# Kernel optimization log

Measured on AMD Instinct MI355X. Metric: run time of the kernel, lower is better.

Reference implementation:

```python
import jax, jax.numpy as jnp
import numpy as np

B, T, C = 8, 1024, 2048  # batch, seq_len (<= T_MAX=1024), n_embd == dim_att


def setup_inputs() -> dict:
    key = jax.random.key(0)
    ks = jax.random.split(key, 10)
    inp = {
        "x": jax.random.normal(ks[0], (B, T, C), dtype=jnp.float32),
        "time_decay": jax.random.normal(ks[1], (C,), dtype=jnp.float32),
        "time_first": jax.random.normal(ks[2], (C,), dtype=jnp.float32),
        "time_mix_k": jax.random.uniform(ks[3], (C,), dtype=jnp.float32),
        "time_mix_v": jax.random.uniform(ks[4], (C,), dtype=jnp.float32),
        "time_mix_r": jax.random.uniform(ks[5], (C,), dtype=jnp.float32),
        "Wk": jax.random.normal(ks[6], (C, C), dtype=jnp.float32) / np.sqrt(C),
        "Wv": jax.random.normal(ks[7], (C, C), dtype=jnp.float32) / np.sqrt(C),
        "Wr": jax.random.normal(ks[8], (C, C), dtype=jnp.float32) / np.sqrt(C),
        "Wo": jax.random.normal(ks[9], (C, C), dtype=jnp.float32) / np.sqrt(C),
    }
    return inp


def _wkv(time_decay, time_first, k, v):
    # Numerically-stabilized RWKV linear-attention recurrence (rwkv_linear_attention_cpu).
    # k, v: [B, T, C]; state tracked in float32.
    w = -jnp.exp(time_decay.astype(jnp.float32))  # [C]
    u = time_first.astype(jnp.float32)            # [C]
    kf = k.astype(jnp.float32)
    vf = v.astype(jnp.float32)

    def step(carry, kv):
        num, den, mx = carry           # each [B, C]
        kt, vt = kv                    # each [B, C]
        max_out = jnp.maximum(mx, kt + u)
        e1 = jnp.exp(mx - max_out)
        e2 = jnp.exp(kt + u - max_out)
        out = (e1 * num + e2 * vt) / (e1 * den + e2)
        max_st = jnp.maximum(mx + w, kt)
        e1s = jnp.exp(mx + w - max_st)
        e2s = jnp.exp(kt - max_st)
        return (e1s * num + e2s * vt, e1s * den + e2s, max_st), out

    Bn, Tn, Cn = k.shape
    init = (jnp.zeros((Bn, Cn), jnp.float32),
            jnp.zeros((Bn, Cn), jnp.float32),
            jnp.full((Bn, Cn), -1e38, jnp.float32))
    kT = jnp.swapaxes(kf, 0, 1)  # [T, B, C]
    vT = jnp.swapaxes(vf, 0, 1)
    _, outs = jax.lax.scan(step, init, (kT, vT))
    return jnp.swapaxes(outs, 0, 1).astype(k.dtype)  # [B, T, C]


def reference(x, time_decay, time_first, time_mix_k, time_mix_v, time_mix_r, Wk, Wv, Wr, Wo):
    # time_shift: shift sequence right by one, zero at t=0
    shifted = jnp.pad(x, ((0, 0), (1, 0), (0, 0)))[:, :-1]
    xk = x * time_mix_k + shifted * (1.0 - time_mix_k)
    xv = x * time_mix_v + shifted * (1.0 - time_mix_v)
    xr = x * time_mix_r + shifted * (1.0 - time_mix_r)
    k = jnp.einsum('btc,dc->btd', xk, Wk)
    v = jnp.einsum('btc,dc->btd', xv, Wv)
    r = jnp.einsum('btc,dc->btd', xr, Wr)
    sr = jax.nn.sigmoid(r)
    rwkv = _wkv(time_decay, time_first, k, v)
    return jnp.einsum('btd,cd->btc', sr * rwkv, Wo)
```

## Files before the change

kernel.cpp:

```cpp
#include <hip/hip_runtime.h>
#include <stdint.h>

#define B_DIM 8
#define T_DIM 1024
#define C_DIM 2048
#define M_DIM (B_DIM * T_DIM)
#define SEG   32
#define SEGL  (T_DIM / SEG)

typedef __bf16 bf16x8 __attribute__((ext_vector_type(8)));
typedef __bf16 bf16x4 __attribute__((ext_vector_type(4)));
typedef float  f32x4  __attribute__((ext_vector_type(4)));

__device__ __forceinline__ void gld_lds16(const void* g, void* l) {
    __builtin_amdgcn_global_load_lds((__attribute__((address_space(1))) void*)g,
                                     (__attribute__((address_space(3))) void*)l,
                                     16, 0, 0);
}

__global__ __launch_bounds__(256) void cast_w_kernel(
    const float* __restrict__ w0, const float* __restrict__ w1,
    const float* __restrict__ w2, const float* __restrict__ w3,
    __bf16* __restrict__ dst) {
    const float* srcs[4] = {w0, w1, w2, w3};
    const float* s = srcs[blockIdx.y];
    __bf16* d = dst + (size_t)blockIdx.y * (size_t)C_DIM * C_DIM;
    const size_t i = ((size_t)blockIdx.x * 256 + threadIdx.x) * 4;
    f32x4 v = *(const f32x4*)(s + i);
    bf16x4 o;
#pragma unroll
    for (int j = 0; j < 4; ++j) o[j] = (__bf16)v[j];
    *(bf16x4*)(d + i) = o;
}

__global__ __launch_bounds__(256) void mix4_kernel(
    const float* __restrict__ x,
    const float* __restrict__ mk, const float* __restrict__ mv,
    const float* __restrict__ mr,
    __bf16* __restrict__ xk, __bf16* __restrict__ xv, __bf16* __restrict__ xr) {
    const size_t idx = ((size_t)blockIdx.x * 256 + threadIdx.x) * 4;
    const int c = (int)(idx & (C_DIM - 1));
    const int t = (int)((idx >> 11) & (T_DIM - 1));

    f32x4 xc = *(const f32x4*)(x + idx);
    f32x4 sh = {0.f, 0.f, 0.f, 0.f};
    if (t != 0) sh = *(const f32x4*)(x + idx - C_DIM);
    f32x4 k4 = *(const f32x4*)(mk + c);
    f32x4 v4 = *(const f32x4*)(mv + c);
    f32x4 r4 = *(const f32x4*)(mr + c);

    bf16x4 ok, ov, orr;
#pragma unroll
    for (int j = 0; j < 4; ++j) {
        float xx = xc[j], ss = sh[j];
        ok[j]  = (__bf16)(xx * k4[j] + ss * (1.f - k4[j]));
        ov[j]  = (__bf16)(xx * v4[j] + ss * (1.f - v4[j]));
        orr[j] = (__bf16)(xx * r4[j] + ss * (1.f - r4[j]));
    }
    *(bf16x4*)(xk + idx) = ok;
    *(bf16x4*)(xv + idx) = ov;
    *(bf16x4*)(xr + idx) = orr;
}

#define VMCNT(N) asm volatile("s_waitcnt vmcnt(" #N ")" ::: "memory")
#define LGKM0()  do { asm volatile("s_waitcnt lgkmcnt(0)" ::: "memory"); \
                      __builtin_amdgcn_sched_barrier(0); } while (0)

#define MFMA4(mi, a)                                                              \
    acc[mi][0] = __builtin_amdgcn_mfma_f32_16x16x32_bf16(a, b0, acc[mi][0], 0, 0, 0); \
    acc[mi][1] = __builtin_amdgcn_mfma_f32_16x16x32_bf16(a, b1, acc[mi][1], 0, 0, 0); \
    acc[mi][2] = __builtin_amdgcn_mfma_f32_16x16x32_bf16(a, b2, acc[mi][2], 0, 0, 0); \
    acc[mi][3] = __builtin_amdgcn_mfma_f32_16x16x32_bf16(a, b3, acc[mi][3], 0, 0, 0)

#define STAGE_A(TT, NB)                                                           \
    do { const __bf16* g_ = Ag + (TT) * 32;                                       \
         __bf16* l_ = lA + (NB) * 8192;                                           \
         gld_lds16(g_, l_);                                                       \
         gld_lds16(g_ + (size_t)128 * C_DIM, l_ + 4096); } while (0)

#define STAGE_B(TT, NB)                                                           \
    do { const __bf16* g_ = Bg + (TT) * 32;                                       \
         __bf16* l_ = lB + (NB) * 8192;                                           \
         gld_lds16(g_, l_);                                                       \
         gld_lds16(g_ + (size_t)128 * C_DIM, l_ + 4096); } while (0)

#define GBLOCK(BUF, DO_STAGE, TT, DO_VM, VM)                                      \
  { const char* pa = fA + (BUF) * 16384;                                          \
    const char* pb = fB + (BUF) * 16384;                                          \
    bf16x8 af0 = *(const bf16x8*)(pa);                                            \
    bf16x8 af1 = *(const bf16x8*)(pa + 1024);                                     \
    bf16x8 af2 = *(const bf16x8*)(pa + 2048);                                     \
    bf16x8 af3 = *(const bf16x8*)(pa + 3072);                                     \
    bf16x8 b0  = *(const bf16x8*)(pb);                                            \
    bf16x8 b1  = *(const bf16x8*)(pb + 1024);                                     \
    bf16x8 b2  = *(const bf16x8*)(pb + 2048);                                     \
    bf16x8 b3  = *(const bf16x8*)(pb + 3072);                                     \
    if (DO_STAGE) { STAGE_A(TT, ((BUF) + 3) & 3); }                               \
    __builtin_amdgcn_s_barrier();                                                 \
    LGKM0();                                                                      \
    __builtin_amdgcn_s_setprio(1);                                                \
    MFMA4(0, af0); MFMA4(1, af1); MFMA4(2, af2); MFMA4(3, af3);                   \
    __builtin_amdgcn_s_setprio(0);                                                \
    __builtin_amdgcn_s_barrier();                                                 \
    af0 = *(const bf16x8*)(pa + 4096);                                            \
    af1 = *(const bf16x8*)(pa + 5120);                                            \
    af2 = *(const bf16x8*)(pa + 6144);                                            \
    af3 = *(const bf16x8*)(pa + 7168);                                            \
    if (DO_STAGE) { STAGE_B(TT, ((BUF) + 3) & 3); }                               \
    __builtin_amdgcn_s_barrier();                                                 \
    LGKM0();                                                                      \
    __builtin_amdgcn_s_setprio(1);                                                \
    MFMA4(4, af0); MFMA4(5, af1); MFMA4(6, af2); MFMA4(7, af3);                   \
    __builtin_amdgcn_s_setprio(0);                                                \
    if (DO_VM) { VMCNT(VM); }                                                     \
    __builtin_amdgcn_s_barrier();                                                 \
  }

template <bool OUTF32>
__global__ __launch_bounds__(512, 2) void gemm256_bt(
    const __bf16* __restrict__ A, const __bf16* __restrict__ W,
    void* __restrict__ Cout) {
    __shared__ __align__(16) __bf16 sA[4 * 8192];
    __shared__ __align__(16) __bf16 sB[4 * 8192];

    const int tid  = threadIdx.x;
    const int lane = tid & 63;
    const int wave = tid >> 6;
    const int wr   = wave >> 2;
    const int wc   = wave & 3;

    const int bid = blockIdx.x;
    const int wid = (bid & 7) * 32 + (bid >> 3);
    const int m_blk = wid & 31;
    const int n_blk = wid >> 5;
    const int row0 = m_blk * 256;
    const int col0 = n_blk * 256;

    const int u  = tid >> 3;
    const int z  = (tid & 7) ^ (u & 7);
    const int srow = 2 * u + (z >> 2);
    const int scol = (z & 3) * 8;
    const __bf16* Ag = A + (size_t)(row0 + srow) * C_DIM + scol;
    const __bf16* Bg = W + (size_t)(col0 + srow) * C_DIM + scol;
    __bf16* lA = sA + wave * 512;
    __bf16* lB = sB + wave * 512;

    const int l15 = lane & 15, l2 = l15 >> 1;
    const int lbyte = l2 * 128 + ((((lane >> 4) + ((lane & 1) << 2)) ^ l2) << 4);
    const char* fA = (const char*)sA + wr * 8192 + lbyte;
    const char* fB = (const char*)sB + wc * 4096 + lbyte;

    f32x4 acc[8][4] = {};

    const int NT = C_DIM / 32;

    STAGE_A(0, 0); STAGE_B(0, 0);
    STAGE_A(1, 1); STAGE_B(1, 1);
    STAGE_A(2, 2); STAGE_B(2, 2);
    VMCNT(8);
    __builtin_amdgcn_s_barrier();

#pragma unroll 1
    for (int t = 0; t < NT - 4; t += 4) {
        GBLOCK(0, true, t + 3, true, 8);
        GBLOCK(1, true, t + 4, true, 8);
        GBLOCK(2, true, t + 5, true, 8);
        GBLOCK(3, true, t + 6, true, 8);
    }
    GBLOCK(0, true,  NT - 1, true, 8);
    GBLOCK(1, false, 0,      true, 4);
    GBLOCK(2, false, 0,      true, 0);
    GBLOCK(3, false, 0,      false, 0);

    const int crow = (lane >> 4) * 4;
#pragma unroll
    for (int mf = 0; mf < 8; ++mf)
#pragma unroll
        for (int jf = 0; jf < 4; ++jf)
#pragma unroll
            for (int r = 0; r < 4; ++r) {
                const int row = row0 + wr * 128 + mf * 16 + crow + r;
                const int col = col0 + wc * 64 + jf * 16 + l15;
                if constexpr (OUTF32) {
                    ((float*)Cout)[(size_t)row * C_DIM + col] = acc[mf][jf][r];
                } else {
                    ((__bf16*)Cout)[(size_t)row * C_DIM + col] = (__bf16)acc[mf][jf][r];
                }
            }
}

__global__ __launch_bounds__(256) void wkv_pass1(
    const __bf16* __restrict__ kbuf, const __bf16* __restrict__ vbuf,
    const float* __restrict__ td,
    float* __restrict__ st_num, float* __restrict__ st_den,
    float* __restrict__ st_m) {
    const int c = blockIdx.x * 256 + threadIdx.x;
    const int b = blockIdx.y;
    const int s = blockIdx.z;
    const size_t base = (size_t)b * T_DIM * C_DIM + (size_t)s * SEGL * C_DIM + c;

    const float w = -__expf(td[c]);
    float num = 0.f, den = 0.f, mx = -1e38f;

    for (int t0 = 0; t0 < SEGL; t0 += 8) {
        float kt[8], vt[8];
#pragma unroll
        for (int j = 0; j < 8; ++j) {
            const size_t idx = base + (size_t)(t0 + j) * C_DIM;
            kt[j] = (float)kbuf[idx];
            vt[j] = (float)vbuf[idx];
        }
#pragma unroll
        for (int j = 0; j < 8; ++j) {
            float ms  = fmaxf(mx + w, kt[j]);
            float e1s = __expf(mx + w - ms);
            float e2s = __expf(kt[j] - ms);
            num = e1s * num + e2s * vt[j];
            den = e1s * den + e2s;
            mx  = ms;
        }
    }
    const size_t sidx = (size_t)s * (B_DIM * C_DIM) + (size_t)b * C_DIM + c;
    st_num[sidx] = num;
    st_den[sidx] = den;
    st_m[sidx]   = mx;
}

__global__ __launch_bounds__(256) void wkv_pass2(
    const float* __restrict__ td,
    float* __restrict__ st_num, float* __restrict__ st_den,
    float* __restrict__ st_m) {
    const int bc = blockIdx.x * 256 + threadIdx.x;
    const int c  = bc & (C_DIM - 1);
    const float w = -__expf(td[c]);
    const float wL = w * SEGL;

    float num = 0.f, den = 0.f, mx = -1e38f;
    for (int s = 0; s < SEG; ++s) {
        const size_t sidx = (size_t)s * (B_DIM * C_DIM) + bc;
        float na = st_num[sidx], da = st_den[sidx], ma = st_m[sidx];
        st_num[sidx] = num; st_den[sidx] = den; st_m[sidx] = mx;
        float md = mx + wL;
        float mc = fmaxf(md, ma);
        float e1 = __expf(md - mc);
        float e2 = __expf(ma - mc);
        num = e1 * num + e2 * na;
        den = e1 * den + e2 * da;
        mx  = mc;
    }
}

__global__ __launch_bounds__(256) void wkv_pass3(
    const __bf16* __restrict__ kbuf, const __bf16* __restrict__ vbuf,
    const __bf16* __restrict__ rbuf, const float* __restrict__ td,
    const float* __restrict__ tf,
    const float* __restrict__ st_num, const float* __restrict__ st_den,
    const float* __restrict__ st_m, __bf16* __restrict__ abuf) {
    const int c = blockIdx.x * 256 + threadIdx.x;
    const int b = blockIdx.y;
    const int s = blockIdx.z;
    const size_t base = (size_t)b * T_DIM * C_DIM + (size_t)s * SEGL * C_DIM + c;

    const float w = -__expf(td[c]);
    const float u = tf[c];
    const size_t sidx = (size_t)s * (B_DIM * C_DIM) + (size_t)b * C_DIM + c;
    float num = st_num[sidx], den = st_den[sidx], mx = st_m[sidx];

    for (int t0 = 0; t0 < SEGL; t0 += 8) {
        float kt[8], vt[8], rt[8];
#pragma unroll
        for (int j = 0; j < 8; ++j) {
            const size_t idx = base + (size_t)(t0 + j) * C_DIM;
            kt[j] = (float)kbuf[idx];
            vt[j] = (float)vbuf[idx];
            rt[j] = (float)rbuf[idx];
        }
#pragma unroll
        for (int j = 0; j < 8; ++j) {
            float mo  = fmaxf(mx, kt[j] + u);
            float e1  = __expf(mx - mo);
            float e2  = __expf(kt[j] + u - mo);
            float out = (e1 * num + e2 * vt[j]) / (e1 * den + e2);

            float ms  = fmaxf(mx + w, kt[j]);
            float e1s = __expf(mx + w - ms);
            float e2s = __expf(kt[j] - ms);
            num = e1s * num + e2s * vt[j];
            den = e1s * den + e2s;
            mx  = ms;

            float sr = 1.f / (1.f + __expf(-rt[j]));
            abuf[base + (size_t)(t0 + j) * C_DIM] = (__bf16)(sr * out);
        }
    }
}

extern "C" void kernel_launch(void* const* d_in, const int* in_sizes, int n_in,
                              void* d_out, int out_size, void* d_ws, size_t ws_size,
                              hipStream_t stream) {
    (void)in_sizes; (void)n_in; (void)out_size; (void)ws_size;
    const float* x  = (const float*)d_in[0];
    const float* td = (const float*)d_in[1];
    const float* tf = (const float*)d_in[2];
    const float* mk = (const float*)d_in[3];
    const float* mv = (const float*)d_in[4];
    const float* mr = (const float*)d_in[5];
    const float* Wk = (const float*)d_in[6];
    const float* Wv = (const float*)d_in[7];
    const float* Wr = (const float*)d_in[8];
    const float* Wo = (const float*)d_in[9];
    float* out = (float*)d_out;

    const size_t WN = (size_t)C_DIM * C_DIM;
    const size_t n  = (size_t)M_DIM * C_DIM;

    __bf16* Wb  = (__bf16*)d_ws;
    __bf16* Wkb = Wb;
    __bf16* Wvb = Wb + WN;
    __bf16* Wrb = Wb + 2 * WN;
    __bf16* Wob = Wb + 3 * WN;
    __bf16* xk  = Wb + 4 * WN;
    __bf16* xv  = xk + n;
    __bf16* xr  = xv + n;
    __bf16* kb  = xr + n;
    __bf16* vb  = xk;
    __bf16* rb  = xv;
    __bf16* ab  = xr;

    float* st_num = (float*)d_ws;
    float* st_den = st_num + (size_t)SEG * B_DIM * C_DIM;
    float* st_m   = st_den + (size_t)SEG * B_DIM * C_DIM;

    cast_w_kernel<<<dim3((unsigned)(WN / 4 / 256), 4), 256, 0, stream>>>(
        Wk, Wv, Wr, Wo, Wb);

    mix4_kernel<<<dim3((unsigned)(n / 4 / 256)), 256, 0, stream>>>(
        x, mk, mv, mr, xk, xv, xr);

    dim3 ggrid((M_DIM / 256) * (C_DIM / 256));
    gemm256_bt<false><<<ggrid, 512, 0, stream>>>(xk, Wkb, kb);
    gemm256_bt<false><<<ggrid, 512, 0, stream>>>(xv, Wvb, vb);
    gemm256_bt<false><<<ggrid, 512, 0, stream>>>(xr, Wrb, rb);

    dim3 wgrid(C_DIM / 256, B_DIM, SEG);
    wkv_pass1<<<wgrid, 256, 0, stream>>>(kb, vb, td, st_num, st_den, st_m);
    wkv_pass2<<<dim3(B_DIM * C_DIM / 256), 256, 0, stream>>>(
        td, st_num, st_den, st_m);
    wkv_pass3<<<wgrid, 256, 0, stream>>>(kb, vb, rb, td, tf,
                                         st_num, st_den, st_m, ab);

    gemm256_bt<true><<<ggrid, 512, 0, stream>>>(ab, Wob, out);
}
```

Before: 530.3 us.

## Restructure GEMM main loop into double-buffered K=64 tiles with new LDS swizzle

Replaces the four-stage K=32 ring buffer in the bf16 GEMM with a two-buffer scheme where each buffer holds a K=64 tile split into two K=32 halves. Global-to-LDS loads are interleaved across the four MFMA quarters of each tile, and the shared-memory layout and read offsets use a new XOR swizzle. The aim is to keep global loads in flight across more MFMA work, issue fewer vmcnt waits, and cut LDS bank conflicts. In exchange the prefetch distance is shorter in stages, and the hand-written wait counts and barrier ordering have to be exactly right.

Measured after the change: 500.5 us. 5.6% less time.

```diff
diff --git a/kernel.cpp b/kernel.cpp
--- a/kernel.cpp
+++ b/kernel.cpp
@@ -62,66 +62,78 @@
     *(bf16x4*)(xr + idx) = orr;
 }
 
-#define VMCNT(N) asm volatile("s_waitcnt vmcnt(" #N ")" ::: "memory")
 #define LGKM0()  do { asm volatile("s_waitcnt lgkmcnt(0)" ::: "memory"); \
                       __builtin_amdgcn_sched_barrier(0); } while (0)
-
-#define MFMA4(mi, a)                                                              \
-    acc[mi][0] = __builtin_amdgcn_mfma_f32_16x16x32_bf16(a, b0, acc[mi][0], 0, 0, 0); \
-    acc[mi][1] = __builtin_amdgcn_mfma_f32_16x16x32_bf16(a, b1, acc[mi][1], 0, 0, 0); \
-    acc[mi][2] = __builtin_amdgcn_mfma_f32_16x16x32_bf16(a, b2, acc[mi][2], 0, 0, 0); \
-    acc[mi][3] = __builtin_amdgcn_mfma_f32_16x16x32_bf16(a, b3, acc[mi][3], 0, 0, 0)
-
-#define STAGE_A(TT, NB)                                                           \
-    do { const __bf16* g_ = Ag + (TT) * 32;                                       \
-         __bf16* l_ = lA + (NB) * 8192;                                           \
-         gld_lds16(g_, l_);                                                       \
-         gld_lds16(g_ + (size_t)128 * C_DIM, l_ + 4096); } while (0)
-
-#define STAGE_B(TT, NB)                                                           \
-    do { const __bf16* g_ = Bg + (TT) * 32;                                       \
-         __bf16* l_ = lB + (NB) * 8192;                                           \
-         gld_lds16(g_, l_);                                                       \
-         gld_lds16(g_ + (size_t)128 * C_DIM, l_ + 4096); } while (0)
-
-#define GBLOCK(BUF, DO_STAGE, TT, DO_VM, VM)                                      \
-  { const char* pa = fA + (BUF) * 16384;                                          \
-    const char* pb = fB + (BUF) * 16384;                                          \
-    bf16x8 af0 = *(const bf16x8*)(pa);                                            \
-    bf16x8 af1 = *(const bf16x8*)(pa + 1024);                                     \
-    bf16x8 af2 = *(const bf16x8*)(pa + 2048);                                     \
-    bf16x8 af3 = *(const bf16x8*)(pa + 3072);                                     \
-    bf16x8 b0  = *(const bf16x8*)(pb);                                            \
-    bf16x8 b1  = *(const bf16x8*)(pb + 1024);                                     \
-    bf16x8 b2  = *(const bf16x8*)(pb + 2048);                                     \
-    bf16x8 b3  = *(const bf16x8*)(pb + 3072);                                     \
-    if (DO_STAGE) { STAGE_A(TT, ((BUF) + 3) & 3); }                               \
-    __builtin_amdgcn_s_barrier();                                                 \
-    LGKM0();                                                                      \
-    __builtin_amdgcn_s_setprio(1);                                                \
-    MFMA4(0, af0); MFMA4(1, af1); MFMA4(2, af2); MFMA4(3, af3);                   \
-    __builtin_amdgcn_s_setprio(0);                                                \
-    __builtin_amdgcn_s_barrier();                                                 \
-    af0 = *(const bf16x8*)(pa + 4096);                                            \
-    af1 = *(const bf16x8*)(pa + 5120);                                            \
-    af2 = *(const bf16x8*)(pa + 6144);                                            \
-    af3 = *(const bf16x8*)(pa + 7168);                                            \
-    if (DO_STAGE) { STAGE_B(TT, ((BUF) + 3) & 3); }                               \
-    __builtin_amdgcn_s_barrier();                                                 \
-    LGKM0();                                                                      \
-    __builtin_amdgcn_s_setprio(1);                                                \
-    MFMA4(4, af0); MFMA4(5, af1); MFMA4(6, af2); MFMA4(7, af3);                   \
-    __builtin_amdgcn_s_setprio(0);                                                \
-    if (DO_VM) { VMCNT(VM); }                                                     \
-    __builtin_amdgcn_s_barrier();                                                 \
+#define VMC(N)   asm volatile("s_waitcnt vmcnt(" #N ")" ::: "memory")
+
+#define MF1(mi, jj, AV, BV) \
+    acc[mi][jj] = __builtin_amdgcn_mfma_f32_16x16x32_bf16(AV, BV, acc[mi][jj], 0, 0, 0)
+
+#define MFQ(MB)                                                              \
+    __builtin_amdgcn_s_setprio(1);                                           \
+    MF1(MB+0,0,aF[0],bF[0]); MF1(MB+0,1,aF[0],bF[1]);                        \
+    MF1(MB+0,2,aF[0],bF[2]); MF1(MB+0,3,aF[0],bF[3]);                        \
+    MF1(MB+1,0,aF[1],bF[0]); MF1(MB+1,1,aF[1],bF[1]);                        \
+    MF1(MB+1,2,aF[1],bF[2]); MF1(MB+1,3,aF[1],bF[3]);                        \
+    MF1(MB+2,0,aF[2],bF[0]); MF1(MB+2,1,aF[2],bF[1]);                        \
+    MF1(MB+2,2,aF[2],bF[2]); MF1(MB+2,3,aF[2],bF[3]);                        \
+    MF1(MB+3,0,aF[3],bF[0]); MF1(MB+3,1,aF[3],bF[1]);                        \
+    MF1(MB+3,2,aF[3],bF[2]); MF1(MB+3,3,aF[3],bF[3]);                        \
+    __builtin_amdgcn_s_setprio(0)
+
+#define RD_A4(DB, KS, MH)                                                    \
+    aF[0] = *(const bf16x8*)(sA + ((DB)*2+(KS))*8192 + wrA + ((MH)*4+0)*512 + rdOf); \
+    aF[1] = *(const bf16x8*)(sA + ((DB)*2+(KS))*8192 + wrA + ((MH)*4+1)*512 + rdOf); \
+    aF[2] = *(const bf16x8*)(sA + ((DB)*2+(KS))*8192 + wrA + ((MH)*4+2)*512 + rdOf); \
+    aF[3] = *(const bf16x8*)(sA + ((DB)*2+(KS))*8192 + wrA + ((MH)*4+3)*512 + rdOf)
+
+#define RD_B4(DB, KS)                                                        \
+    bF[0] = *(const bf16x8*)(sB + ((DB)*2+(KS))*8192 + wcB + 0*512 + rdOf);  \
+    bF[1] = *(const bf16x8*)(sB + ((DB)*2+(KS))*8192 + wcB + 1*512 + rdOf);  \
+    bF[2] = *(const bf16x8*)(sB + ((DB)*2+(KS))*8192 + wcB + 2*512 + rdOf);  \
+    bF[3] = *(const bf16x8*)(sB + ((DB)*2+(KS))*8192 + wcB + 3*512 + rdOf)
+
+#define STG_A(T, KH, DBX)                                                    \
+    gld_lds16(AgS + (size_t)(T)*64 + (KH)*32,                                \
+              sA + (DBX)*16384 + (KH)*8192 + wvOf);                          \
+    gld_lds16(AgS + (size_t)(T)*64 + (KH)*32 + (size_t)128*C_DIM,            \
+              sA + (DBX)*16384 + (KH)*8192 + 4096 + wvOf)
+#define STG_B(T, KH, DBX)                                                    \
+    gld_lds16(BgS + (size_t)(T)*64 + (KH)*32,                                \
+              sB + (DBX)*16384 + (KH)*8192 + wvOf);                          \
+    gld_lds16(BgS + (size_t)(T)*64 + (KH)*32 + (size_t)128*C_DIM,            \
+              sB + (DBX)*16384 + (KH)*8192 + 4096 + wvOf)
+
+#define KTILE(DB, S1, S2, S3, S4, VM4)                                       \
+  {                                                                          \
+    RD_B4(DB,0); RD_A4(DB,0,0); S1;                                          \
+    __builtin_amdgcn_sched_barrier(0);                                       \
+    __builtin_amdgcn_s_barrier(); LGKM0();                                   \
+    MFQ(0);                                                                  \
+    __builtin_amdgcn_s_barrier();                                            \
+    RD_A4(DB,0,1); S2;                                                       \
+    __builtin_amdgcn_sched_barrier(0);                                       \
+    __builtin_amdgcn_s_barrier(); LGKM0();                                   \
+    MFQ(4);                                                                  \
+    __builtin_amdgcn_s_barrier();                                            \
+    RD_B4(DB,1); RD_A4(DB,1,0); S3;                                          \
+    __builtin_amdgcn_sched_barrier(0);                                       \
+    __builtin_amdgcn_s_barrier(); LGKM0();                                   \
+    MFQ(0);                                                                  \
+    __builtin_amdgcn_s_barrier();                                            \
+    RD_A4(DB,1,1); S4; VM4;                                                  \
+    __builtin_amdgcn_sched_barrier(0);                                       \
+    __builtin_amdgcn_s_barrier(); LGKM0();                                   \
+    MFQ(4);                                                                  \
+    __builtin_amdgcn_s_barrier();                                            \
   }
 
 template <bool OUTF32>
 __global__ __launch_bounds__(512, 2) void gemm256_bt(
     const __bf16* __restrict__ A, const __bf16* __restrict__ W,
     void* __restrict__ Cout) {
-    __shared__ __align__(16) __bf16 sA[4 * 8192];
-    __shared__ __align__(16) __bf16 sB[4 * 8192];
+    __shared__ __align__(16) __bf16 sA[32768];
+    __shared__ __align__(16) __bf16 sB[32768];
 
     const int tid  = threadIdx.x;
     const int lane = tid & 63;
@@ -136,41 +148,37 @@
     const int row0 = m_blk * 256;
     const int col0 = n_blk * 256;
 
-    const int u  = tid >> 3;
-    const int z  = (tid & 7) ^ (u & 7);
-    const int srow = 2 * u + (z >> 2);
-    const int scol = (z & 3) * 8;
-    const __bf16* Ag = A + (size_t)(row0 + srow) * C_DIM + scol;
-    const __bf16* Bg = W + (size_t)(col0 + srow) * C_DIM + scol;
-    __bf16* lA = sA + wave * 512;
-    __bf16* lB = sB + wave * 512;
-
-    const int l15 = lane & 15, l2 = l15 >> 1;
-    const int lbyte = l2 * 128 + ((((lane >> 4) + ((lane & 1) << 2)) ^ l2) << 4);
-    const char* fA = (const char*)sA + wr * 8192 + lbyte;
-    const char* fB = (const char*)sB + wc * 4096 + lbyte;
-
-    f32x4 acc[8][4] = {};
-
-    const int NT = C_DIM / 32;
-
-    STAGE_A(0, 0); STAGE_B(0, 0);
-    STAGE_A(1, 1); STAGE_B(1, 1);
-    STAGE_A(2, 2); STAGE_B(2, 2);
-    VMCNT(8);
+    const int srow = tid >> 2;
+    const int swkg = (tid & 3) ^ (srow & 3) ^ ((srow >> 2) & 3);
+    const __bf16* AgS = A + (size_t)(row0 + srow) * C_DIM + swkg * 8;
+    const __bf16* BgS = W + (size_t)(col0 + srow) * C_DIM + swkg * 8;
+    const int wvOf = wave * 512;
+
+    const int l15 = lane & 15;
+    const int q   = lane >> 4;
+    const int rdOf = l15 * 32 + ((q ^ (l15 & 3) ^ ((l15 >> 2) & 3)) * 8);
+    const int wrA  = wr * 4096;
+    const int wcB  = wc * 2048;
+
+    f32x4  acc[8][4] = {};
+    bf16x8 aF[4], bF[4];
+
+    STG_A(0, 0, 0); STG_B(0, 0, 0); STG_A(0, 1, 0); STG_B(0, 1, 0);
+    STG_B(1, 0, 1); STG_A(1, 0, 1); STG_B(1, 1, 1);
+    VMC(6);
+    __builtin_amdgcn_sched_barrier(0);
     __builtin_amdgcn_s_barrier();
 
 #pragma unroll 1
-    for (int t = 0; t < NT - 4; t += 4) {
-        GBLOCK(0, true, t + 3, true, 8);
-        GBLOCK(1, true, t + 4, true, 8);
-        GBLOCK(2, true, t + 5, true, 8);
-        GBLOCK(3, true, t + 6, true, 8);
-    }
-    GBLOCK(0, true,  NT - 1, true, 8);
-    GBLOCK(1, false, 0,      true, 4);
-    GBLOCK(2, false, 0,      true, 0);
-    GBLOCK(3, false, 0,      false, 0);
+    for (int p = 0; p < 15; ++p) {
+        const int t = 2 * p;
+        KTILE(0, STG_A(t + 1, 1, 1), STG_B(t + 2, 0, 0),
+                 STG_A(t + 2, 0, 0), STG_B(t + 2, 1, 0), VMC(6));
+        KTILE(1, STG_A(t + 2, 1, 0), STG_B(t + 3, 0, 1),
+                 STG_A(t + 3, 0, 1), STG_B(t + 3, 1, 1), VMC(6));
+    }
+    KTILE(0, STG_A(31, 1, 1), , , , VMC(0));
+    KTILE(1, , , , , );
 
     const int crow = (lane >> 4) * 4;
 #pragma unroll
```
